# Performance work log

Measured on AMD Instinct MI355X. Metric: run time of the kernel, lower is better.

Reference implementation:

```python
import jax, jax.numpy as jnp
import numpy as np

N_NODES = 50000
N_EDGES = 600000
N_GRAPHS = 2048
EMB = 128
N_LAYERS = 3
ATOM_FEATS, ATOM_VOCAB = 9, 100
BOND_FEATS, BOND_VOCAB, BOND_DIM = 3, 8, 3


def setup_inputs() -> dict:
    key = jax.random.key(0)
    ks = jax.random.split(key, 10)
    x = jax.random.randint(ks[0], (N_NODES, ATOM_FEATS), 0, ATOM_VOCAB)
    edge_index = jax.random.randint(ks[1], (2, N_EDGES), 0, N_NODES)
    edge_attr = jax.random.randint(ks[2], (N_EDGES, BOND_FEATS), 0, BOND_VOCAB)
    batch = jnp.sort(jax.random.randint(ks[3], (N_NODES,), 0, N_GRAPHS))
    s = 1.0 / np.sqrt(EMB).astype(np.float32)
    atom_emb = jax.random.normal(ks[4], (ATOM_FEATS, ATOM_VOCAB, EMB), jnp.float32) * 0.1
    bond_emb = jax.random.normal(ks[5], (N_LAYERS, BOND_FEATS, BOND_VOCAB, BOND_DIM), jnp.float32) * 0.1
    W = jax.random.normal(ks[6], (N_LAYERS, BOND_DIM, EMB, EMB), jnp.float32) * s
    b = jnp.zeros((N_LAYERS, BOND_DIM, EMB), jnp.float32)
    fc1_w = jax.random.normal(ks[7], (EMB, EMB), jnp.float32) * s
    fc1_b = jnp.zeros((EMB,), jnp.float32)
    fc2_w = jax.random.normal(ks[8], (EMB, 1), jnp.float32) * s
    fc2_b = jnp.zeros((1,), jnp.float32)
    return dict(x=x, edge_index=edge_index, edge_attr=edge_attr, batch=batch,
                atom_emb=atom_emb, bond_emb=bond_emb, W=W, b=b,
                fc1_w=fc1_w, fc1_b=fc1_b, fc2_w=fc2_w, fc2_b=fc2_b)


def reference(x, edge_index, edge_attr, batch, atom_emb, bond_emb, W, b,
              fc1_w, fc1_b, fc2_w, fc2_b):
    src, dst = edge_index[0], edge_index[1]
    n = x.shape[0]
    # AtomEncoder: sum of per-column embedding lookups -> [N, EMB]
    h = atom_emb[0][x[:, 0]]
    for c in range(1, ATOM_FEATS):
        h = h + atom_emb[c][x[:, c]]
    for layer in range(N_LAYERS):
        # BondEncoder: [E, BOND_DIM] edge weights (one scalar channel per conv)
        ew = bond_emb[layer, 0][edge_attr[:, 0]]
        for c in range(1, BOND_FEATS):
            ew = ew + bond_emb[layer, c][edge_attr[:, c]]
        # Three parallel GCNConv(normalize=False): linear, gather src, edge-weight, scatter-add to dst
        msg = jnp.zeros((edge_index.shape[1], EMB), h.dtype)
        for k in range(BOND_DIM):
            xw = h @ W[layer, k]              # [N, EMB]
            msg = msg + ew[:, k:k + 1] * xw[src]   # [E, EMB]
        agg = jax.ops.segment_sum(msg, dst, num_segments=n)
        hn = agg + jnp.sum(b[layer], axis=0)  # sum of the three conv biases
        if layer < N_LAYERS - 1:
            hn = jax.nn.relu(hn)              # dropout is identity at eval
        h = hn + h                            # residual
    # global_mean_pool
    sums = jax.ops.segment_sum(h, batch, num_segments=N_GRAPHS)
    counts = jax.ops.segment_sum(jnp.ones((n,), h.dtype), batch, num_segments=N_GRAPHS)
    hg = sums / jnp.maximum(counts, 1.0)[:, None]
    return (hg @ fc1_w + fc1_b) @ fc2_w + fc2_b   # [N_GRAPHS, 1]
```

## Files before the change

kernel.cpp:

```cpp
#include <hip/hip_runtime.h>

#define N_NODES 50000
#define N_EDGES 600000
#define N_GRAPHS 2048
#define EMB 128
#define TDIM 384
#define TS_LD 392
#define HN (N_NODES * EMB)
#define GROWS 64

#define EPB 2048
#define NBLKA ((N_EDGES + EPB - 1) / EPB)
#define NCOARSE ((N_NODES + 255) / 256)
#define SCAN_TOT (NCOARSE * NBLKA)
#define SC2_NB ((SCAN_TOT + 255) / 256)

#define PRE_ATOM_NB 8334
#define PRE_CNT_NB NBLKA
#define PRE_WCONV_NB 384
#define PRE_GB_NB 131

typedef __attribute__((ext_vector_type(8))) short bf16x8;
typedef __attribute__((ext_vector_type(4))) float f32x4;
#define MFMA_BF16(a, b, c) __builtin_amdgcn_mfma_f32_16x16x32_bf16(a, b, c, 0, 0, 0)

#define AS1 __attribute__((address_space(1)))
#define AS3 __attribute__((address_space(3)))
__device__ inline void gl_lds16(const void* g, void* l) {
  __builtin_amdgcn_global_load_lds((const AS1 void*)g, (AS3 void*)l, 16, 0, 0);
}

__device__ inline unsigned short f2bf(float f) {
  unsigned int u = __float_as_uint(f);
  u += 0x7fffu + ((u >> 16) & 1u);
  return (unsigned short)(u >> 16);
}
__device__ inline float bf2f(unsigned short b) {
  return __uint_as_float(((unsigned int)b) << 16);
}
__device__ inline bf16x8 pack8(float4 lo, float4 hi) {
  bf16x8 r;
  r[0] = (short)f2bf(lo.x); r[1] = (short)f2bf(lo.y);
  r[2] = (short)f2bf(lo.z); r[3] = (short)f2bf(lo.w);
  r[4] = (short)f2bf(hi.x); r[5] = (short)f2bf(hi.y);
  r[6] = (short)f2bf(hi.z); r[7] = (short)f2bf(hi.w);
  return r;
}

__global__ __launch_bounds__(384) void k_pre(const int* __restrict__ x,
                                             const float* __restrict__ atom_emb,
                                             unsigned short* __restrict__ h_bf,
                                             const int* __restrict__ ei,
                                             int* __restrict__ ghist,
                                             const float* __restrict__ W,
                                             unsigned short* __restrict__ wt,
                                             const int* __restrict__ batch,
                                             int* __restrict__ gs) {
  __shared__ float sb[6 * 1280];
  int blk = blockIdx.x;
  if (blk < PRE_ATOM_NB) {
    const int wv = threadIdx.x >> 6;
    const int lane = threadIdx.x & 63;
    int n = blk * 6 + wv;
    if (n < N_NODES) {
      const int nu = __builtin_amdgcn_readfirstlane(n);
      const int* xr = x + nu * 9;
      int ix[9];
#pragma unroll
      for (int c = 0; c < 9; ++c) ix[c] = xr[c];
      float* wbase = sb + wv * 1280;
      const int half = lane >> 5;
      const int sub16 = lane & 31;
#pragma unroll
      for (int j = 0; j < 4; ++j) {
        int c = 2 * j + half;
        const float* g = atom_emb + (size_t)(c * 100 + ix[c]) * EMB + sub16 * 4;
        gl_lds16(g, wbase + j * 256);
      }
      {
        const float* g = atom_emb + (size_t)(8 * 100 + ix[8]) * EMB + sub16 * 4;
        gl_lds16(g, wbase + 1024);
      }
      asm volatile("s_waitcnt vmcnt(0)" ::: "memory");
      float2 acc = {0.f, 0.f};
#pragma unroll
      for (int c = 0; c < 9; ++c) {
        float2 v = *(const float2*)(wbase + c * 128 + lane * 2);
        acc.x += v.x; acc.y += v.y;
      }
      *(ushort2*)(h_bf + (size_t)nu * EMB + lane * 2) = ushort2{f2bf(acc.x), f2bf(acc.y)};
    }
    return;
  }
  blk -= PRE_ATOM_NB;
  if (blk < PRE_CNT_NB) {
    int* h = (int*)sb;
    const int t = threadIdx.x;
    if (t < 256) h[t] = 0;
    __syncthreads();
    const int base = blk * EPB;
#pragma unroll
    for (int k = 0; k < 6; ++k) {
      int o = k * 384 + t;
      int e = base + o;
      if (o < EPB && e < N_EDGES) atomicAdd(&h[ei[N_EDGES + e] >> 8], 1);
    }
    __syncthreads();
    if (t < NCOARSE) ghist[(size_t)t * NBLKA + blk] = h[t];
    return;
  }
  blk -= PRE_CNT_NB;
  if (blk < PRE_WCONV_NB) {
    int layer = blk >> 7, c = blk & 127, k = threadIdx.x;
    float v = W[(((layer * 3 + (k >> 7)) * 128) + (k & 127)) * 128 + c];
    wt[(size_t)blk * 384 + k] = f2bf(v);
    return;
  }
  blk -= PRE_WCONV_NB;
  {
    int i = blk * 384 + threadIdx.x;
    if (i < N_NODES) {
      int b = batch[i];
      int bp = (i == 0) ? -1 : batch[i - 1];
      for (int g = bp + 1; g <= b; ++g) gs[g] = i;
      if (i == N_NODES - 1) {
        for (int g = b + 1; g <= N_GRAPHS; ++g) gs[g] = N_NODES;
      }
    }
  }
}

__global__ __launch_bounds__(256) void k_gscan_a(int* __restrict__ ghist,
                                                 int* __restrict__ partials) {
  __shared__ int s[256];
  const int t = threadIdx.x;
  const int i = blockIdx.x * 256 + t;
  int v = (i < SCAN_TOT) ? ghist[i] : 0;
  s[t] = v;
  __syncthreads();
  for (int off = 1; off < 256; off <<= 1) {
    int u = (t >= off) ? s[t - off] : 0;
    __syncthreads();
    s[t] += u;
    __syncthreads();
  }
  if (i < SCAN_TOT) ghist[i] = s[t] - v;
  if (t == 255) partials[blockIdx.x] = s[255];
}

__global__ __launch_bounds__(256) void k_gscan_b(int* __restrict__ partials,
                                                 int* __restrict__ bucket_base,
                                                 int* __restrict__ row_start) {
  __shared__ int s[256];
  const int t = threadIdx.x;
  int v = (t < SC2_NB) ? partials[t] : 0;
  s[t] = v;
  __syncthreads();
  for (int off = 1; off < 256; off <<= 1) {
    int u = (t >= off) ? s[t - off] : 0;
    __syncthreads();
    s[t] += u;
    __syncthreads();
  }
  if (t < SC2_NB) partials[t] = s[t] - v;
  if (t == 0) { bucket_base[NCOARSE] = N_EDGES; row_start[N_NODES] = N_EDGES; }
}

__global__ __launch_bounds__(256) void k_gscan_c(int* __restrict__ ghist,
                                                 const int* __restrict__ partials,
                                                 int* __restrict__ bucket_base) {
  const int i = blockIdx.x * 256 + threadIdx.x;
  if (i < SCAN_TOT) {
    int g = ghist[i] + partials[blockIdx.x];
    ghist[i] = g;
    int d = i / NBLKA;
    if (i - d * NBLKA == 0) bucket_base[d] = g;
  }
}

__global__ __launch_bounds__(256) void k_coarse(const int* __restrict__ ei,
                                                const int* __restrict__ ea,
                                                const int* __restrict__ ghist,
                                                int2* __restrict__ tmp) {
  __shared__ int cnt[256];
  const int t = threadIdx.x;
  cnt[t] = 0;
  __syncthreads();
  const int base = blockIdx.x * EPB;
#pragma unroll
  for (int k = 0; k < 8; ++k) {
    int e = base + k * 256 + t;
    if (e < N_EDGES) {
      int dst = ei[N_EDGES + e];
      int d = dst >> 8;
      int r = atomicAdd(&cnt[d], 1);
      int pos = ghist[(size_t)d * NBLKA + blockIdx.x] + r;
      int eap = ea[e * 3 + 0] | (ea[e * 3 + 1] << 3) | (ea[e * 3 + 2] << 6);
      tmp[pos] = int2{dst | (eap << 16), ei[e]};
    }
  }
}

__global__ __launch_bounds__(256) void k_fine(const int2* __restrict__ tmp,
                                              const int* __restrict__ bucket_base,
                                              int* __restrict__ row_start,
                                              int2* __restrict__ sorted_se) {
  __shared__ int h[256];
  __shared__ int s[256];
  __shared__ int ex[256];
  const int t = threadIdx.x;
  const int d = blockIdx.x;
  const int b0 = bucket_base[d], b1 = bucket_base[d + 1];
  h[t] = 0;
  __syncthreads();
  for (int i = b0 + t; i < b1; i += 256) atomicAdd(&h[tmp[i].x & 255], 1);
  __syncthreads();
  s[t] = h[t];
  __syncthreads();
  for (int off = 1; off < 256; off <<= 1) {
    int v = (t >= off) ? s[t - off] : 0;
    __syncthreads();
    s[t] += v;
    __syncthreads();
  }
  ex[t] = s[t] - h[t];
  int node = d * 256 + t;
  if (node < N_NODES) row_start[node] = b0 + ex[t];
  h[t] = 0;
  __syncthreads();
  for (int i = b0 + t; i < b1; i += 256) {
    int2 r = tmp[i];
    int f = r.x & 255;
    int pos = b0 + ex[f] + atomicAdd(&h[f], 1);
    sorted_se[pos] = int2{r.y, (r.x >> 16) & 511};
  }
}

__global__ __launch_bounds__(256) void k_agg(const int2* __restrict__ sorted_se,
                                             const int* __restrict__ row_start,
                                             const float* __restrict__ bl,
                                             const unsigned short* __restrict__ h_bf,
                                             unsigned short* __restrict__ t_bf) {
  __shared__ float4 combo[512];
  const int node = blockIdx.x * 16 + (threadIdx.x >> 4);
  const int sub = threadIdx.x & 15;
  const int beg = row_start[node], end = row_start[node + 1];
  int e = beg;
  const int full_end = beg + ((end - beg) & ~7);
  int2 se[8];
  if (e < full_end) {
#pragma unroll
    for (int j = 0; j < 8; ++j) se[j] = sorted_se[e + j];
  }
  for (int c = threadIdx.x; c < 512; c += 256) {
    int a0 = c & 7, a1 = (c >> 3) & 7, a2 = (c >> 6) & 7;
    combo[c] = float4{bl[a0 * 3 + 0] + bl[24 + a1 * 3 + 0] + bl[48 + a2 * 3 + 0],
                      bl[a0 * 3 + 1] + bl[24 + a1 * 3 + 1] + bl[48 + a2 * 3 + 1],
                      bl[a0 * 3 + 2] + bl[24 + a1 * 3 + 2] + bl[48 + a2 * 3 + 2], 0.f};
  }
  __syncthreads();
  float4 l0 = {0.f, 0.f, 0.f, 0.f}, h0 = l0;
  float4 l1 = l0, h1 = l0;
  float4 l2 = l0, h2 = l0;
  while (e < full_end) {
    bf16x8 u[8];
#pragma unroll
    for (int j = 0; j < 8; ++j)
      u[j] = *(const bf16x8*)(h_bf + (size_t)se[j].x * EMB + sub * 8);
    e += 8;
    int2 se_n[8];
    const bool more = (e < full_end);
    if (more) {
#pragma unroll
      for (int j = 0; j < 8; ++j) se_n[j] = sorted_se[e + j];
    }
#pragma unroll
    for (int j = 0; j < 8; ++j) {
      float4 w = combo[se[j].y];
      float4 vlo = {bf2f((unsigned short)u[j][0]), bf2f((unsigned short)u[j][1]),
                    bf2f((unsigned short)u[j][2]), bf2f((unsigned short)u[j][3])};
      float4 vhi = {bf2f((unsigned short)u[j][4]), bf2f((unsigned short)u[j][5]),
                    bf2f((unsigned short)u[j][6]), bf2f((unsigned short)u[j][7])};
      l0 += vlo * w.x; h0 += vhi * w.x;
      l1 += vlo * w.y; h1 += vhi * w.y;
      l2 += vlo * w.z; h2 += vhi * w.z;
    }
    if (more) {
#pragma unroll
      for (int j = 0; j < 8; ++j) se[j] = se_n[j];
    }
  }
  if (e < end) {
    int2 st[8];
#pragma unroll
    for (int j = 0; j < 8; ++j) {
      int idx = e + j;
      st[j] = sorted_se[idx < end ? idx : end - 1];
    }
    bf16x8 u[8];
#pragma unroll
    for (int j = 0; j < 8; ++j)
      u[j] = *(const bf16x8*)(h_bf + (size_t)st[j].x * EMB + sub * 8);
#pragma unroll
    for (int j = 0; j < 8; ++j) {
      float4 w = (e + j < end) ? combo[st[j].y] : float4{0.f, 0.f, 0.f, 0.f};
      float4 vlo = {bf2f((unsigned short)u[j][0]), bf2f((unsigned short)u[j][1]),
                    bf2f((unsigned short)u[j][2]), bf2f((unsigned short)u[j][3])};
      float4 vhi = {bf2f((unsigned short)u[j][4]), bf2f((unsigned short)u[j][5]),
                    bf2f((unsigned short)u[j][6]), bf2f((unsigned short)u[j][7])};
      l0 += vlo * w.x; h0 += vhi * w.x;
      l1 += vlo * w.y; h1 += vhi * w.y;
      l2 += vlo * w.z; h2 += vhi * w.z;
    }
  }
  size_t base = (size_t)node * TDIM + sub * 8;
  *(bf16x8*)(t_bf + base)       = pack8(l0, h0);
  *(bf16x8*)(t_bf + base + 128) = pack8(l1, h1);
  *(bf16x8*)(t_bf + base + 256) = pack8(l2, h2);
}

__global__ __launch_bounds__(512) void k_gemm(const unsigned short* __restrict__ t_bf,
                                              const unsigned short* __restrict__ wt,
                                              const float* __restrict__ bl,
                                              const unsigned short* __restrict__ h_in_bf,
                                              unsigned short* __restrict__ h_out_bf,
                                              int do_relu) {
  __shared__ unsigned short ts[GROWS * TS_LD];
  const int nb = blockIdx.x * GROWS;
  for (int i = threadIdx.x; i < GROWS * 48; i += 512) {
    int r = i / 48, cc = i % 48;
    bf16x8 v = {};
    int row = nb + r;
    if (row < N_NODES) v = *(const bf16x8*)(t_bf + (size_t)row * TDIM + cc * 8);
    *(bf16x8*)(ts + r * TS_LD + cc * 8) = v;
  }
  __syncthreads();

  const int wv = threadIdx.x >> 6;
  const int lane = threadIdx.x & 63;
  const int m = lane & 15;
  const int kq = lane >> 4;
  const int c = wv * 16 + m;

  const unsigned short* pB = wt + (size_t)c * TDIM + kq * 8;
  bf16x8 B[12];
#pragma unroll
  for (int kc = 0; kc < 12; ++kc) B[kc] = *(const bf16x8*)(pB + kc * 32);

  const float bias = bl[c] + bl[128 + c] + bl[256 + c];

#pragma unroll
  for (int rt = 0; rt < 4; ++rt) {
    const unsigned short* pA = ts + (rt * 16 + m) * TS_LD + kq * 8;
    bf16x8 A[12];
#pragma unroll
    for (int kc = 0; kc < 12; ++kc) A[kc] = *(const bf16x8*)(pA + kc * 32);
    f32x4 acc = {0.f, 0.f, 0.f, 0.f};
#pragma unroll
    for (int kc = 0; kc < 12; ++kc) acc = MFMA_BF16(A[kc], B[kc], acc);
#pragma unroll
    for (int r = 0; r < 4; ++r) {
      int row = nb + rt * 16 + kq * 4 + r;
      if (row < N_NODES) {
        size_t idx = (size_t)row * EMB + c;
        float v = acc[r] + bias;
        if (do_relu) v = fmaxf(v, 0.f);
        float hn = bf2f(h_in_bf[idx]) + v;
        h_out_bf[idx] = f2bf(hn);
      }
    }
  }
}

__global__ __launch_bounds__(128) void k_head(const unsigned short* __restrict__ h_bf,
                                              const int* __restrict__ gs,
                                              const float* __restrict__ fc1_w,
                                              const float* __restrict__ fc1_b,
                                              const float* __restrict__ fc2_w,
                                              const float* __restrict__ fc2_b,
                                              float* __restrict__ out) {
  __shared__ float hg[EMB];
  __shared__ float red[EMB];
  int g = blockIdx.x, e = threadIdx.x;
  int ns = gs[g], ne = gs[g + 1];
  float acc = 0.f;
  for (int n = ns; n < ne; ++n) acc += bf2f(h_bf[(size_t)n * EMB + e]);
  float cnt = fmaxf((float)(ne - ns), 1.f);
  hg[e] = acc / cnt;
  __syncthreads();
  float a2 = fc1_b[e];
  for (int j = 0; j < EMB; ++j) a2 += hg[j] * fc1_w[j * EMB + e];
  red[e] = a2 * fc2_w[e];
  __syncthreads();
  for (int s = 64; s > 0; s >>= 1) {
    if (e < s) red[e] += red[e + s];
    __syncthreads();
  }
  if (e == 0) out[g] = red[0] + fc2_b[0];
}

extern "C" void kernel_launch(void* const* d_in, const int* in_sizes, int n_in,
                              void* d_out, int out_size, void* d_ws, size_t ws_size,
                              hipStream_t stream) {
  const int*   x        = (const int*)d_in[0];
  const int*   ei       = (const int*)d_in[1];
  const int*   ea       = (const int*)d_in[2];
  const int*   batch    = (const int*)d_in[3];
  const float* atom_emb = (const float*)d_in[4];
  const float* bond_emb = (const float*)d_in[5];
  const float* W        = (const float*)d_in[6];
  const float* b        = (const float*)d_in[7];
  const float* fc1_w    = (const float*)d_in[8];
  const float* fc1_b    = (const float*)d_in[9];
  const float* fc2_w    = (const float*)d_in[10];
  const float* fc2_b    = (const float*)d_in[11];
  float* out = (float*)d_out;

  char* p = (char*)d_ws;
  auto alloc = [&](size_t bytes) { char* r = p; p += (bytes + 255) & ~(size_t)255; return r; };
  unsigned short* h0_bf      = (unsigned short*)alloc((size_t)HN * 2);
  unsigned short* h1_bf      = (unsigned short*)alloc((size_t)HN * 2);
  unsigned short* t_bf       = (unsigned short*)alloc((size_t)N_NODES * TDIM * 2);
  unsigned short* wt         = (unsigned short*)alloc((size_t)3 * 128 * TDIM * 2);
  int*            gs         = (int*)alloc((size_t)(N_GRAPHS + 1) * 4);
  int*            row_start  = (int*)alloc((size_t)(N_NODES + 1) * 4);
  int*            ghist      = (int*)alloc((size_t)SCAN_TOT * 4);
  int*            spart      = (int*)alloc((size_t)SC2_NB * 4);
  int*            bucket_base= (int*)alloc((size_t)(NCOARSE + 1) * 4);
  int2*           tmp_se     = (int2*)alloc((size_t)N_EDGES * 8);
  int2*           sorted_se  = (int2*)alloc((size_t)(N_EDGES + 8) * 8);

  const int pre_blocks = PRE_ATOM_NB + PRE_CNT_NB + PRE_WCONV_NB + PRE_GB_NB;
  k_pre<<<pre_blocks, 384, 0, stream>>>(x, atom_emb, h0_bf, ei, ghist, W, wt, batch, gs);
  k_gscan_a<<<SC2_NB, 256, 0, stream>>>(ghist, spart);
  k_gscan_b<<<1, 256, 0, stream>>>(spart, bucket_base, row_start);
  k_gscan_c<<<SC2_NB, 256, 0, stream>>>(ghist, spart, bucket_base);
  k_coarse<<<NBLKA, 256, 0, stream>>>(ei, ea, ghist, tmp_se);
  k_fine<<<NCOARSE, 256, 0, stream>>>(tmp_se, bucket_base, row_start, sorted_se);

  unsigned short* hib = h0_bf;
  unsigned short* hob = h1_bf;
  const int gemm_blocks = (N_NODES + GROWS - 1) / GROWS;
  for (int layer = 0; layer < 3; ++layer) {
    k_agg<<<N_NODES / 16, 256, 0, stream>>>(sorted_se, row_start, bond_emb + layer * 72,
                                            hib, t_bf);
    k_gemm<<<gemm_blocks, 512, 0, stream>>>(
        t_bf, wt + (size_t)layer * 128 * TDIM, b + layer * 3 * EMB,
        hib, hob, layer < 2 ? 1 : 0);
    unsigned short* tb = hib; hib = hob; hob = tb;
  }

  k_head<<<N_GRAPHS, 128, 0, stream>>>(hib, gs, fc1_w, fc1_b, fc2_w, fc2_b, out);
}
```

Measured before the change: 315.1 us.

## Split atom encoder across coarse and fine sort kernels; prefetch GEMM weights early

Moves the atom-embedding lookup out of the precompute kernel and splits it in two halves, appended as extra blocks to the edge-sort kernels k_coarse and k_fine, which have few blocks and otherwise leave the GPU underfilled. This is meant to fill those kernels with independent work and shorten k_pre. It also issues the GEMM weight-fragment and bias loads before the LDS staging loop so their latency overlaps it. The risk is extra LDS per block in the sort kernels and changed scheduling of those small kernels.

```diff
diff --git a/kernel.cpp b/kernel.cpp
--- a/kernel.cpp
+++ b/kernel.cpp
@@ -15,10 +15,12 @@
 #define SCAN_TOT (NCOARSE * NBLKA)
 #define SC2_NB ((SCAN_TOT + 255) / 256)
 
-#define PRE_ATOM_NB 8334
 #define PRE_CNT_NB NBLKA
 #define PRE_WCONV_NB 384
 #define PRE_GB_NB 131
+
+#define ATOM_HALF 25000
+#define ATOM_NB 6250
 
 typedef __attribute__((ext_vector_type(8))) short bf16x8;
 typedef __attribute__((ext_vector_type(4))) float f32x4;
@@ -47,54 +49,51 @@
   return r;
 }
 
-__global__ __launch_bounds__(384) void k_pre(const int* __restrict__ x,
-                                             const float* __restrict__ atom_emb,
-                                             unsigned short* __restrict__ h_bf,
-                                             const int* __restrict__ ei,
+__device__ inline void atom_block(int nbase, int blk, const int* __restrict__ x,
+                                  const float* __restrict__ atom_emb,
+                                  unsigned short* __restrict__ h_bf, float* sb) {
+  const int wv = threadIdx.x >> 6;
+  const int lane = threadIdx.x & 63;
+  int n = nbase + blk * 4 + wv;
+  if (n < N_NODES) {
+    const int nu = __builtin_amdgcn_readfirstlane(n);
+    const int* xr = x + nu * 9;
+    int ix[9];
+#pragma unroll
+    for (int c = 0; c < 9; ++c) ix[c] = xr[c];
+    float* wbase = sb + wv * 1280;
+    const int half = lane >> 5;
+    const int sub16 = lane & 31;
+#pragma unroll
+    for (int j = 0; j < 4; ++j) {
+      int c = 2 * j + half;
+      const float* g = atom_emb + (size_t)(c * 100 + ix[c]) * EMB + sub16 * 4;
+      gl_lds16(g, wbase + j * 256);
+    }
+    {
+      const float* g = atom_emb + (size_t)(8 * 100 + ix[8]) * EMB + sub16 * 4;
+      gl_lds16(g, wbase + 1024);
+    }
+    asm volatile("s_waitcnt vmcnt(0)" ::: "memory");
+    float2 acc = {0.f, 0.f};
+#pragma unroll
+    for (int c = 0; c < 9; ++c) {
+      float2 v = *(const float2*)(wbase + c * 128 + lane * 2);
+      acc.x += v.x; acc.y += v.y;
+    }
+    *(ushort2*)(h_bf + (size_t)nu * EMB + lane * 2) = ushort2{f2bf(acc.x), f2bf(acc.y)};
+  }
+}
+
+__global__ __launch_bounds__(384) void k_pre(const int* __restrict__ ei,
                                              int* __restrict__ ghist,
                                              const float* __restrict__ W,
                                              unsigned short* __restrict__ wt,
                                              const int* __restrict__ batch,
                                              int* __restrict__ gs) {
-  __shared__ float sb[6 * 1280];
+  __shared__ int h[256];
   int blk = blockIdx.x;
-  if (blk < PRE_ATOM_NB) {
-    const int wv = threadIdx.x >> 6;
-    const int lane = threadIdx.x & 63;
-    int n = blk * 6 + wv;
-    if (n < N_NODES) {
-      const int nu = __builtin_amdgcn_readfirstlane(n);
-      const int* xr = x + nu * 9;
-      int ix[9];
-#pragma unroll
-      for (int c = 0; c < 9; ++c) ix[c] = xr[c];
-      float* wbase = sb + wv * 1280;
-      const int half = lane >> 5;
-      const int sub16 = lane & 31;
-#pragma unroll
-      for (int j = 0; j < 4; ++j) {
-        int c = 2 * j + half;
-        const float* g = atom_emb + (size_t)(c * 100 + ix[c]) * EMB + sub16 * 4;
-        gl_lds16(g, wbase + j * 256);
-      }
-      {
-        const float* g = atom_emb + (size_t)(8 * 100 + ix[8]) * EMB + sub16 * 4;
-        gl_lds16(g, wbase + 1024);
-      }
-      asm volatile("s_waitcnt vmcnt(0)" ::: "memory");
-      float2 acc = {0.f, 0.f};
-#pragma unroll
-      for (int c = 0; c < 9; ++c) {
-        float2 v = *(const float2*)(wbase + c * 128 + lane * 2);
-        acc.x += v.x; acc.y += v.y;
-      }
-      *(ushort2*)(h_bf + (size_t)nu * EMB + lane * 2) = ushort2{f2bf(acc.x), f2bf(acc.y)};
-    }
-    return;
-  }
-  blk -= PRE_ATOM_NB;
   if (blk < PRE_CNT_NB) {
-    int* h = (int*)sb;
     const int t = threadIdx.x;
     if (t < 256) h[t] = 0;
     __syncthreads();
@@ -181,8 +180,16 @@
 __global__ __launch_bounds__(256) void k_coarse(const int* __restrict__ ei,
                                                 const int* __restrict__ ea,
                                                 const int* __restrict__ ghist,
-                                                int2* __restrict__ tmp) {
-  __shared__ int cnt[256];
+                                                int2* __restrict__ tmp,
+                                                const int* __restrict__ x,
+                                                const float* __restrict__ atom_emb,
+                                                unsigned short* __restrict__ h_bf) {
+  __shared__ float sb[4 * 1280];
+  if (blockIdx.x >= NBLKA) {
+    atom_block(0, blockIdx.x - NBLKA, x, atom_emb, h_bf, sb);
+    return;
+  }
+  int* cnt = (int*)sb;
   const int t = threadIdx.x;
   cnt[t] = 0;
   __syncthreads();
@@ -204,10 +211,18 @@
 __global__ __launch_bounds__(256) void k_fine(const int2* __restrict__ tmp,
                                               const int* __restrict__ bucket_base,
                                               int* __restrict__ row_start,
-                                              int2* __restrict__ sorted_se) {
-  __shared__ int h[256];
-  __shared__ int s[256];
-  __shared__ int ex[256];
+                                              int2* __restrict__ sorted_se,
+                                              const int* __restrict__ x,
+                                              const float* __restrict__ atom_emb,
+                                              unsigned short* __restrict__ h_bf) {
+  __shared__ float sb[4 * 1280];
+  if (blockIdx.x >= NCOARSE) {
+    atom_block(ATOM_HALF, blockIdx.x - NCOARSE, x, atom_emb, h_bf, sb);
+    return;
+  }
+  int* h = (int*)sb;
+  int* s = h + 256;
+  int* ex = s + 256;
   const int t = threadIdx.x;
   const int d = blockIdx.x;
   const int b0 = bucket_base[d], b1 = bucket_base[d + 1];
@@ -327,6 +342,18 @@
                                               int do_relu) {
   __shared__ unsigned short ts[GROWS * TS_LD];
   const int nb = blockIdx.x * GROWS;
+  const int wv = threadIdx.x >> 6;
+  const int lane = threadIdx.x & 63;
+  const int m = lane & 15;
+  const int kq = lane >> 4;
+  const int c = wv * 16 + m;
+
+  const unsigned short* pB = wt + (size_t)c * TDIM + kq * 8;
+  bf16x8 B[12];
+#pragma unroll
+  for (int kc = 0; kc < 12; ++kc) B[kc] = *(const bf16x8*)(pB + kc * 32);
+  const float bias = bl[c] + bl[128 + c] + bl[256 + c];
+
   for (int i = threadIdx.x; i < GROWS * 48; i += 512) {
     int r = i / 48, cc = i % 48;
     bf16x8 v = {};
@@ -335,19 +362,6 @@
     *(bf16x8*)(ts + r * TS_LD + cc * 8) = v;
   }
   __syncthreads();
-
-  const int wv = threadIdx.x >> 6;
-  const int lane = threadIdx.x & 63;
-  const int m = lane & 15;
-  const int kq = lane >> 4;
-  const int c = wv * 16 + m;
-
-  const unsigned short* pB = wt + (size_t)c * TDIM + kq * 8;
-  bf16x8 B[12];
-#pragma unroll
-  for (int kc = 0; kc < 12; ++kc) B[kc] = *(const bf16x8*)(pB + kc * 32);
-
-  const float bias = bl[c] + bl[128 + c] + bl[256 + c];
 
 #pragma unroll
   for (int rt = 0; rt < 4; ++rt) {
@@ -430,13 +444,15 @@
   int2*           tmp_se     = (int2*)alloc((size_t)N_EDGES * 8);
   int2*           sorted_se  = (int2*)alloc((size_t)(N_EDGES + 8) * 8);
 
-  const int pre_blocks = PRE_ATOM_NB + PRE_CNT_NB + PRE_WCONV_NB + PRE_GB_NB;
-  k_pre<<<pre_blocks, 384, 0, stream>>>(x, atom_emb, h0_bf, ei, ghist, W, wt, batch, gs);
+  const int pre_blocks = PRE_CNT_NB + PRE_WCONV_NB + PRE_GB_NB;
+  k_pre<<<pre_blocks, 384, 0, stream>>>(ei, ghist, W, wt, batch, gs);
   k_gscan_a<<<SC2_NB, 256, 0, stream>>>(ghist, spart);
   k_gscan_b<<<1, 256, 0, stream>>>(spart, bucket_base, row_start);
   k_gscan_c<<<SC2_NB, 256, 0, stream>>>(ghist, spart, bucket_base);
-  k_coarse<<<NBLKA, 256, 0, stream>>>(ei, ea, ghist, tmp_se);
-  k_fine<<<NCOARSE, 256, 0, stream>>>(tmp_se, bucket_base, row_start, sorted_se);
+  k_coarse<<<NBLKA + ATOM_NB, 256, 0, stream>>>(ei, ea, ghist, tmp_se,
+                                                x, atom_emb, h0_bf);
+  k_fine<<<NCOARSE + ATOM_NB, 256, 0, stream>>>(tmp_se, bucket_base, row_start, sorted_se,
+                                                x, atom_emb, h0_bf);
 
   unsigned short* hib = h0_bf;
   unsigned short* hob = h1_bf;
```

After: 304.3 us, median of 2. -3.4%, faster.
